# Kernel tuning notes

Hardware: AMD Instinct MI355X
Metric: run time of the kernel (lower is better)

The kernel has to match this reference:

```python
import jax, jax.numpy as jnp
import numpy as np

VOCAB = 50000
D = 32            # hidden_size
OUT = 5           # output_size (sentiment classes)
B = 512           # number of balanced trees
L = 64            # leaves per tree (power of 2)


def setup_inputs() -> dict:
    key = jax.random.key(0)
    ks = jax.random.split(key, 6)
    # scale params down to avoid tanh saturation (original uses xavier init)
    return {
        "word_ids": jax.random.randint(ks[0], (B, L), 0, VOCAB, dtype=jnp.int32),
        "embed": jax.random.normal(ks[1], (VOCAB, D), jnp.float32) * 0.1,
        "V": jax.random.normal(ks[2], (D, 2 * D, 2 * D), jnp.float32) * 0.02,
        "W": jax.random.normal(ks[3], (2 * D, D), jnp.float32) * 0.1,
        "b": jnp.zeros((1, D), jnp.float32),
        "Wout_w": jax.random.normal(ks[4], (OUT, D), jnp.float32) * 0.1,
        "Wout_b": jnp.zeros((OUT,), jnp.float32),
    }


def reference(word_ids, embed, V, W, b, Wout_w, Wout_b):
    # Leaves: embedding lookup. h: [B, n_nodes_at_level, D]
    h = embed[word_ids]                              # [B, L, D]
    all_nodes = [h.reshape(-1, D)]
    n_levels = int(np.log2(h.shape[1]))
    for _ in range(n_levels):
        left = h[:, 0::2]                            # [B, n/2, D]
        right = h[:, 1::2]                           # [B, n/2, D]
        c = jnp.concatenate([left, right], axis=-1)  # [B, n/2, 2D]
        # xVx_k = c @ V_k @ c^T for each slice k of the tensor V
        Vc = jnp.einsum('kjl,bnl->bnkj', V, c)       # [B, n/2, D, 2D]
        xVx = jnp.einsum('bnj,bnkj->bnk', c, Vc)     # [B, n/2, D]
        h = jnp.tanh(xVx + c @ W + b)                # [B, n/2, D]
        all_nodes.append(h.reshape(-1, D))
    nodes = jnp.concatenate(all_nodes, axis=0)       # [B*(2L-1), D]
    logits = nodes @ Wout_w.T + Wout_b               # [B*(2L-1), OUT]
    log_probs = jax.nn.log_softmax(logits, axis=-1)
    roots = h[:, 0, :]                               # [B, D]
    return log_probs, roots
```

## Files before the change

kernel.cpp:

```cpp
#include <hip/hip_runtime.h>

#define OUT_N 5
#define TOTAL_NODES 65024
#define ROOTS_OFF (TOTAL_NODES * OUT_N)

typedef __attribute__((ext_vector_type(8))) short bf16x8;
typedef __attribute__((ext_vector_type(4))) float f32x4;
typedef __attribute__((ext_vector_type(8))) unsigned short ushort8v;
typedef __attribute__((ext_vector_type(4))) unsigned int uint4v;

constexpr int B_BYTES   = 137216;
constexpr int NODE_SZ   = 16128;
constexpr int LEAF_SZ   = 8192;
constexpr int LDS_BIG   = B_BYTES + NODE_SZ + LEAF_SZ;
constexpr int LDS_SMALL = NODE_SZ + LEAF_SZ;

static __device__ __forceinline__ float bf2f(unsigned short u) {
    union { unsigned int i; float f; } v; v.i = ((unsigned int)u) << 16; return v.f;
}
static __device__ __forceinline__ unsigned short f2bf(float f) {
    union { float f; unsigned int i; } v; v.f = f;
    unsigned int r = v.i + 0x7fff + ((v.i >> 16) & 1);
    return (unsigned short)(r >> 16);
}

static __device__ __forceinline__ int naddr32(int R, int c) {
    return R * 128 + (((c + R + (R >> 1)) & 7) << 4);
}
static __device__ __forceinline__ int laddr16(int R, int q) {
    return R * 64 + (((q + R + (R >> 1)) & 3) << 4);
}
static __device__ __forceinline__ void store_h32(char* base, int R, int col, float v) {
    *(float*)(base + naddr32(R, col >> 2) + (col & 3) * 4) = v;
}
static __device__ __forceinline__ void load_crot32(
    const char* base, int Rc, int hi, float* crot)
{
    #pragma unroll
    for (int t = 0; t < 16; ++t) {
        int m = (hi * 2 + t) & 15;
        f32x4 v = *(const f32x4*)(base + naddr32(Rc + (m >> 3), m & 7));
        #pragma unroll
        for (int e = 0; e < 4; ++e) crot[t * 4 + e] = v[e];
    }
}

__global__ __launch_bounds__(64) void bprep_kernel(
    const float* __restrict__ V, const float* __restrict__ W,
    unsigned short* __restrict__ B)
{
    int t = blockIdx.x * 64 + threadIdx.x;
    if (t >= 8576) return;
    int ks = t >> 7, sub = t & 127;
    int n = sub >> 6, lane = sub & 63;
    int hi = lane >> 4, l15 = lane & 15;
    int k = n * 16 + l15;
    const float* Vk = V + (size_t)k * 4096;
    ushort8v o;
    #pragma unroll
    for (int i = 0; i < 8; ++i) {
        int r5 = hi * 8 + i;
        float val;
        if (ks < 2)        { int j = 32 * ks + r5; val = Vk[j * 64 + j]; }
        else if (ks < 64)  { int d = ks >> 1; int j = 32 * (ks & 1) + r5; int l = (j + d) & 63;
                             val = Vk[j * 64 + l] + Vk[l * 64 + j]; }
        else if (ks == 64) { int j = r5; val = Vk[j * 64 + j + 32] + Vk[(j + 32) * 64 + j]; }
        else               { int j = (ks == 65) ? r5 : (32 + r5); val = W[j * 32 + k]; }
        o[i] = f2bf(val);
    }
    *(ushort8v*)(B + (size_t)t * 8) = o;
}

template<int BLDS, int K0, int K1>
static __device__ __forceinline__ f32x4 run1(
    const unsigned short* __restrict__ Bg, const float* crot,
    int lane, int n, f32x4 acc)
{
    extern __shared__ char smem[];
    const int lo = lane * 16 + (n << 10);
    #pragma unroll
    for (int ks = K0; ks < K1; ++ks) {
        uint4v aw;
        #pragma unroll
        for (int q = 0; q < 4; ++q) {
            int i0 = 2 * q, i1 = 2 * q + 1;
            float p0, p1;
            if (ks < 2)       { p0 = crot[32*ks+i0] * crot[32*ks+i0];
                                p1 = crot[32*ks+i1] * crot[32*ks+i1]; }
            else if (ks < 64) { const int bse = 32 * (ks & 1), d = ks >> 1;
                                p0 = crot[bse+i0] * crot[(bse+i0+d)&63];
                                p1 = crot[bse+i1] * crot[(bse+i1+d)&63]; }
            else if (ks == 64){ p0 = crot[i0] * crot[32+i0];
                                p1 = crot[i1] * crot[32+i1]; }
            else if (ks == 65){ p0 = crot[i0];    p1 = crot[i1]; }
            else              { p0 = crot[32+i0]; p1 = crot[32+i1]; }
            unsigned int pk;
            asm("v_cvt_pk_bf16_f32 %0, %1, %2" : "=v"(pk) : "v"(p0), "v"(p1));
            aw[q] = pk;
        }
        bf16x8 afr = __builtin_bit_cast(bf16x8, aw);
        bf16x8 b;
        if constexpr (BLDS) b = *(const bf16x8*)(smem + (ks << 11) + lo);
        else                b = *(const bf16x8*)((const char*)Bg + (ks << 11) + lo);
        acc = __builtin_amdgcn_mfma_f32_16x16x32_bf16(afr, b, acc, 0, 0, 0);
    }
    return acc;
}

template<int BLDS>
static __device__ __attribute__((noinline)) void worker_l1(
    const unsigned short* __restrict__ Bg, const float* __restrict__ bias, int tid)
{
    extern __shared__ char smem[];
    constexpr int NODE = BLDS ? B_BYTES : 0;
    constexpr int LEAF = NODE + NODE_SZ;
    const int lane = tid & 63, w = tid >> 6;
    const int l15 = lane & 15, hi = lane >> 4;
    const int tile = w >> 1, n = w & 1;
    const int tree = tile >> 1, half = tile & 1;

    const int Rc = tree * 64 + half * 32 + 2 * l15;
    float crot[64];
    #pragma unroll
    for (int t = 0; t < 8; ++t) {
        int m = (hi + t) & 7;
        ushort8v v = *(const ushort8v*)(smem + LEAF + laddr16(Rc + (m >> 2), m & 3));
        #pragma unroll
        for (int e = 0; e < 8; ++e) crot[t * 8 + e] = bf2f(v[e]);
    }

    f32x4 a = {0.f,0.f,0.f,0.f};
    a = run1<BLDS, 0, 67>(Bg, crot, lane, n, a);

    float bk = bias[n * 16 + l15];
    #pragma unroll
    for (int r = 0; r < 4; ++r) {
        int R = tree * 63 + half * 16 + hi * 4 + r;
        store_h32(smem + NODE, R, n * 16 + l15, tanhf(a[r] + bk));
    }
    __syncthreads();
}

template<int BLDS>
static __device__ __attribute__((noinline)) void worker_l2(
    const unsigned short* __restrict__ Bg, const float* __restrict__ bias, int tid)
{
    extern __shared__ char smem[];
    constexpr int NODE = BLDS ? B_BYTES : 0;
    constexpr int SCR  = NODE + NODE_SZ;
    const int lane = tid & 63, w = tid >> 6;
    const int l15 = lane & 15, hi = lane >> 4;
    const int tree = w >> 2, n = (w >> 1) & 1, u = w & 1;

    float crot[64];
    load_crot32(smem + NODE, tree * 63 + 2 * l15, hi, crot);

    f32x4 a = {0.f,0.f,0.f,0.f};
    if (u == 0) a = run1<BLDS,  0, 34>(Bg, crot, lane, n, a);
    else        a = run1<BLDS, 34, 67>(Bg, crot, lane, n, a);

    if (u == 1) *(f32x4*)(smem + SCR + ((tree * 2 + n) << 10) + lane * 16) = a;
    __syncthreads();
    if (u == 0) {
        a += *(const f32x4*)(smem + SCR + ((tree * 2 + n) << 10) + lane * 16);
        float bk = bias[n * 16 + l15];
        #pragma unroll
        for (int r = 0; r < 4; ++r) {
            int R = tree * 63 + 32 + hi * 4 + r;
            store_h32(smem + NODE, R, n * 16 + l15, tanhf(a[r] + bk));
        }
    }
    __syncthreads();
}

template<int BLDS>
static __device__ __attribute__((noinline)) void worker_deep(
    const unsigned short* __restrict__ Bg, const float* __restrict__ bias,
    float* __restrict__ roots, int bid, int tid,
    int s, int childb, int outb, bool root)
{
    extern __shared__ char smem[];
    constexpr int NODE = BLDS ? B_BYTES : 0;
    constexpr int SCR  = NODE + NODE_SZ;
    const int lane = tid & 63, w = tid >> 6;
    const int l15 = lane & 15, hi = lane >> 4;
    const int n = w >> 2, u = w & 3;
    const int rptT = 1 << s, rows2 = 2 << s;

    int rc = (l15 < rows2) ? l15 : 0;
    int tree = rc >> s, i = rc & (rptT - 1);
    float crot[64];
    load_crot32(smem + NODE, tree * 63 + childb + 2 * i, hi, crot);

    f32x4 a = {0.f,0.f,0.f,0.f};
    switch (u) {
        case 0:  a = run1<BLDS,  0, 17>(Bg, crot, lane, n, a); break;
        case 1:  a = run1<BLDS, 17, 34>(Bg, crot, lane, n, a); break;
        case 2:  a = run1<BLDS, 34, 50>(Bg, crot, lane, n, a); break;
        default: a = run1<BLDS, 50, 67>(Bg, crot, lane, n, a); break;
    }
    if (u > 0) *(f32x4*)(smem + SCR + ((n * 3 + u - 1) << 10) + lane * 16) = a;
    __syncthreads();
    if (u == 0) {
        #pragma unroll
        for (int v2 = 0; v2 < 3; ++v2)
            a += *(const f32x4*)(smem + SCR + ((n * 3 + v2) << 10) + lane * 16);
        float bk = bias[n * 16 + l15];
        #pragma unroll
        for (int r = 0; r < 4; ++r) {
            int row = hi * 4 + r;
            if (row < rows2) {
                int t2 = row >> s, i2 = row & (rptT - 1);
                float h = tanhf(a[r] + bk);
                store_h32(smem + NODE, t2 * 63 + outb + i2, n * 16 + l15, h);
                if (root) roots[(size_t)(bid * 2 + t2) * 32 + n * 16 + l15] = h;
            }
        }
    }
    __syncthreads();
}

static __device__ __forceinline__ void node_logits32(
    const char* nodebase, int R, const float* __restrict__ Wout_w,
    const float* __restrict__ Wout_b, float* __restrict__ out, size_t g)
{
    float h[32];
    #pragma unroll
    for (int c = 0; c < 8; ++c) {
        f32x4 v = *(const f32x4*)(nodebase + naddr32(R, c));
        #pragma unroll
        for (int e = 0; e < 4; ++e) h[c * 4 + e] = v[e];
    }
    float lg[OUT_N];
    #pragma unroll
    for (int o = 0; o < OUT_N; ++o) {
        const float* ww = Wout_w + o * 32;
        float s = 0.f;
        #pragma unroll
        for (int x = 0; x < 32; ++x) s = fmaf(ww[x], h[x], s);
        lg[o] = s + Wout_b[o];
    }
    float m = lg[0];
    #pragma unroll
    for (int o = 1; o < OUT_N; ++o) m = fmaxf(m, lg[o]);
    float sum = 0.f;
    #pragma unroll
    for (int o = 0; o < OUT_N; ++o) sum += expf(lg[o] - m);
    float lse = m + logf(sum);
    #pragma unroll
    for (int o = 0; o < OUT_N; ++o) out[g * OUT_N + o] = lg[o] - lse;
}

template<int BLDS>
__global__ __launch_bounds__(512, 2) void tree_kernel(
    const int* __restrict__ word_ids, const float* __restrict__ embed,
    const unsigned short* __restrict__ Bg, const float* __restrict__ bias,
    const float* __restrict__ Wout_w, const float* __restrict__ Wout_b,
    float* __restrict__ out)
{
    extern __shared__ char smem[];
    constexpr int NODE = BLDS ? B_BYTES : 0;
    constexpr int LEAF = NODE + NODE_SZ;
    const int tid = threadIdx.x, bid = blockIdx.x;
    float* roots = out + ROOTS_OFF;

    if constexpr (BLDS) {
        const ushort8v* src = (const ushort8v*)Bg;
        #pragma unroll
        for (int r2 = 0; r2 < 16; ++r2) {
            int idx = r2 * 512 + tid;
            *(ushort8v*)(smem + idx * 16) = src[idx];
        }
        int idx = 8192 + tid;
        if (idx < 8576) *(ushort8v*)(smem + idx * 16) = src[idx];
    }

    {
        int rr = tid >> 2, q4 = tid & 3;
        int leaf = bid * 128 + rr;
        int wid = word_ids[leaf];
        const f32x4* ep = (const f32x4*)(embed + (size_t)wid * 32) + q4 * 2;
        f32x4 v0 = ep[0], v1 = ep[1];
        ushort8v o;
        #pragma unroll
        for (int e = 0; e < 4; ++e) { o[e] = f2bf(v0[e]); o[4 + e] = f2bf(v1[e]); }
        *(ushort8v*)(smem + LEAF + laddr16(rr, q4)) = o;

        float lg[OUT_N];
        #pragma unroll
        for (int o5 = 0; o5 < OUT_N; ++o5) {
            const float* ww = Wout_w + o5 * 32 + q4 * 8;
            lg[o5] = ww[0]*v0[0] + ww[1]*v0[1] + ww[2]*v0[2] + ww[3]*v0[3]
                   + ww[4]*v1[0] + ww[5]*v1[1] + ww[6]*v1[2] + ww[7]*v1[3];
        }
        #pragma unroll
        for (int o5 = 0; o5 < OUT_N; ++o5) {
            lg[o5] += __shfl_xor(lg[o5], 1, 64);
            lg[o5] += __shfl_xor(lg[o5], 2, 64);
        }
        if (q4 == 0) {
            #pragma unroll
            for (int o5 = 0; o5 < OUT_N; ++o5) lg[o5] += Wout_b[o5];
            float m = lg[0];
            #pragma unroll
            for (int o5 = 1; o5 < OUT_N; ++o5) m = fmaxf(m, lg[o5]);
            float sum = 0.f;
            #pragma unroll
            for (int o5 = 0; o5 < OUT_N; ++o5) sum += expf(lg[o5] - m);
            float lse = m + logf(sum);
            #pragma unroll
            for (int o5 = 0; o5 < OUT_N; ++o5)
                out[(size_t)leaf * OUT_N + o5] = lg[o5] - lse;
        }
    }
    __syncthreads();

    worker_l1<BLDS>(Bg, bias, tid);
    worker_l2<BLDS>(Bg, bias, tid);
    worker_deep<BLDS>(Bg, bias, roots, bid, tid, 3, 32, 48, false);
    worker_deep<BLDS>(Bg, bias, roots, bid, tid, 2, 48, 56, false);
    worker_deep<BLDS>(Bg, bias, roots, bid, tid, 1, 56, 60, false);
    worker_deep<BLDS>(Bg, bias, roots, bid, tid, 0, 60, 62, true);

    if (tid < 126) {
        int tree = (tid >= 63) ? 1 : 0;
        int r = tid - 63 * tree;
        size_t tg = (size_t)bid * 2 + tree;
        int R = tree * 63 + r;
        size_t g;
        if (r < 32)      g = 32768 + tg * 32 + r;
        else if (r < 48) g = 49152 + tg * 16 + (r - 32);
        else if (r < 56) g = 57344 + tg * 8  + (r - 48);
        else if (r < 60) g = 61440 + tg * 4  + (r - 56);
        else if (r < 62) g = 63488 + tg * 2  + (r - 60);
        else             g = 64512 + tg;
        node_logits32(smem + NODE, R, Wout_w, Wout_b, out, g);
    }
}

extern "C" void kernel_launch(void* const* d_in, const int* in_sizes, int n_in,
                              void* d_out, int out_size, void* d_ws, size_t ws_size,
                              hipStream_t stream)
{
    const int*   word_ids = (const int*)  d_in[0];
    const float* embed    = (const float*)d_in[1];
    const float* V        = (const float*)d_in[2];
    const float* W        = (const float*)d_in[3];
    const float* bvec     = (const float*)d_in[4];
    const float* Wout_w   = (const float*)d_in[5];
    const float* Wout_b   = (const float*)d_in[6];
    float* out = (float*)d_out;

    unsigned short* Bfrag = (unsigned short*)d_ws;

    bprep_kernel<<<134, 64, 0, stream>>>(V, W, Bfrag);

    hipError_t e = hipFuncSetAttribute((const void*)&tree_kernel<1>,
                     hipFuncAttributeMaxDynamicSharedMemorySize, LDS_BIG);
    if (e == hipSuccess) {
        tree_kernel<1><<<256, 512, LDS_BIG, stream>>>(
            word_ids, embed, Bfrag, bvec, Wout_w, Wout_b, out);
    } else {
        tree_kernel<0><<<256, 512, LDS_SMALL, stream>>>(
            word_ids, embed, Bfrag, bvec, Wout_w, Wout_b, out);
    }
}
```

Measured before the change: 31.15 us.

## Double tree-kernel block size and stage V slices through LDS in bprep

Launches the tree kernel with 1024 threads instead of 512. Level 1 now splits its K range across two waves and reduces partials through LDS scratch, while the deeper levels leave the extra waves idle. The bprep kernel now loads each V_k slice into shared memory with coalesced reads before building the fragments, and the leaf embedding gather is spread over 8 lanes per leaf. The global-memory fallback path is removed, so the kernel now depends on the large LDS allocation succeeding. Idle waves in the deep levels add barrier cost, and the added split adds an extra synchronisation.

```diff
diff --git a/kernel.cpp b/kernel.cpp
--- a/kernel.cpp
+++ b/kernel.cpp
@@ -9,11 +9,13 @@
 typedef __attribute__((ext_vector_type(8))) unsigned short ushort8v;
 typedef __attribute__((ext_vector_type(4))) unsigned int uint4v;
 
-constexpr int B_BYTES   = 137216;
-constexpr int NODE_SZ   = 16128;
-constexpr int LEAF_SZ   = 8192;
-constexpr int LDS_BIG   = B_BYTES + NODE_SZ + LEAF_SZ;
-constexpr int LDS_SMALL = NODE_SZ + LEAF_SZ;
+constexpr int B_BYTES = 137216;
+constexpr int NODE_SZ = 16128;
+constexpr int LEAF_SZ = 8192;
+constexpr int NODE = B_BYTES;
+constexpr int LEAF = NODE + NODE_SZ;
+constexpr int SCR  = LEAF;
+constexpr int LDS_BIG = B_BYTES + NODE_SZ + LEAF_SZ;
 
 static __device__ __forceinline__ float bf2f(unsigned short u) {
     union { unsigned int i; float f; } v; v.i = ((unsigned int)u) << 16; return v.f;
@@ -45,36 +47,41 @@
     }
 }
 
-__global__ __launch_bounds__(64) void bprep_kernel(
+__global__ __launch_bounds__(256) void bprep_kernel(
     const float* __restrict__ V, const float* __restrict__ W,
     unsigned short* __restrict__ B)
 {
-    int t = blockIdx.x * 64 + threadIdx.x;
-    if (t >= 8576) return;
-    int ks = t >> 7, sub = t & 127;
-    int n = sub >> 6, lane = sub & 63;
-    int hi = lane >> 4, l15 = lane & 15;
-    int k = n * 16 + l15;
-    const float* Vk = V + (size_t)k * 4096;
-    ushort8v o;
-    #pragma unroll
-    for (int i = 0; i < 8; ++i) {
-        int r5 = hi * 8 + i;
-        float val;
-        if (ks < 2)        { int j = 32 * ks + r5; val = Vk[j * 64 + j]; }
-        else if (ks < 64)  { int d = ks >> 1; int j = 32 * (ks & 1) + r5; int l = (j + d) & 63;
-                             val = Vk[j * 64 + l] + Vk[l * 64 + j]; }
-        else if (ks == 64) { int j = r5; val = Vk[j * 64 + j + 32] + Vk[(j + 32) * 64 + j]; }
-        else               { int j = (ks == 65) ? r5 : (32 + r5); val = W[j * 32 + k]; }
-        o[i] = f2bf(val);
-    }
-    *(ushort8v*)(B + (size_t)t * 8) = o;
-}
-
-template<int BLDS, int K0, int K1>
+    __shared__ float vk[4096];
+    const int tid = threadIdx.x, k = blockIdx.x;
+    #pragma unroll
+    for (int i = 0; i < 4; ++i) {
+        int idx = i * 256 + tid;
+        ((f32x4*)vk)[idx] = ((const f32x4*)(V + (size_t)k * 4096))[idx];
+    }
+    __syncthreads();
+    const int n = k >> 4, l15 = k & 15;
+    for (int jb = tid; jb < 268; jb += 256) {
+        int ks = jb % 67, hi4 = jb / 67;
+        ushort8v o;
+        #pragma unroll
+        for (int i = 0; i < 8; ++i) {
+            int r5 = hi4 * 8 + i;
+            float val;
+            if (ks < 2)        { int j = 32 * ks + r5; val = vk[j * 64 + j]; }
+            else if (ks < 64)  { int d = ks >> 1; int j = 32 * (ks & 1) + r5;
+                                 int l = (j + d) & 63;
+                                 val = vk[j * 64 + l] + vk[l * 64 + j]; }
+            else if (ks == 64) { int j = r5; val = vk[j * 64 + j + 32] + vk[(j + 32) * 64 + j]; }
+            else               { int j = (ks == 65) ? r5 : (32 + r5); val = W[j * 32 + k]; }
+            o[i] = f2bf(val);
+        }
+        *(ushort8v*)(B + (size_t)(ks * 128 + n * 64 + hi4 * 16 + l15) * 8) = o;
+    }
+}
+
+template<int K0, int K1>
 static __device__ __forceinline__ f32x4 run1(
-    const unsigned short* __restrict__ Bg, const float* crot,
-    int lane, int n, f32x4 acc)
+    const float* crot, int lane, int n, f32x4 acc)
 {
     extern __shared__ char smem[];
     const int lo = lane * 16 + (n << 10);
@@ -99,69 +106,99 @@
             aw[q] = pk;
         }
         bf16x8 afr = __builtin_bit_cast(bf16x8, aw);
-        bf16x8 b;
-        if constexpr (BLDS) b = *(const bf16x8*)(smem + (ks << 11) + lo);
-        else                b = *(const bf16x8*)((const char*)Bg + (ks << 11) + lo);
+        bf16x8 b = *(const bf16x8*)(smem + (ks << 11) + lo);
         acc = __builtin_amdgcn_mfma_f32_16x16x32_bf16(afr, b, acc, 0, 0, 0);
     }
     return acc;
 }
 
-template<int BLDS>
+static __device__ __forceinline__ void node_logits32(
+    const char* nodebase, int R, const float* __restrict__ Wout_w,
+    const float* __restrict__ Wout_b, float* __restrict__ out, size_t g)
+{
+    float h[32];
+    #pragma unroll
+    for (int c = 0; c < 8; ++c) {
+        f32x4 v = *(const f32x4*)(nodebase + naddr32(R, c));
+        #pragma unroll
+        for (int e = 0; e < 4; ++e) h[c * 4 + e] = v[e];
+    }
+    float lg[OUT_N];
+    #pragma unroll
+    for (int o = 0; o < OUT_N; ++o) {
+        const float* ww = Wout_w + o * 32;
+        float s = 0.f;
+        #pragma unroll
+        for (int x = 0; x < 32; ++x) s = fmaf(ww[x], h[x], s);
+        lg[o] = s + Wout_b[o];
+    }
+    float m = lg[0];
+    #pragma unroll
+    for (int o = 1; o < OUT_N; ++o) m = fmaxf(m, lg[o]);
+    float sum = 0.f;
+    #pragma unroll
+    for (int o = 0; o < OUT_N; ++o) sum += expf(lg[o] - m);
+    float lse = m + logf(sum);
+    #pragma unroll
+    for (int o = 0; o < OUT_N; ++o) out[g * OUT_N + o] = lg[o] - lse;
+}
+
 static __device__ __attribute__((noinline)) void worker_l1(
-    const unsigned short* __restrict__ Bg, const float* __restrict__ bias, int tid)
-{
-    extern __shared__ char smem[];
-    constexpr int NODE = BLDS ? B_BYTES : 0;
-    constexpr int LEAF = NODE + NODE_SZ;
+    const float* __restrict__ bias, int tid)
+{
+    extern __shared__ char smem[];
     const int lane = tid & 63, w = tid >> 6;
     const int l15 = lane & 15, hi = lane >> 4;
-    const int tile = w >> 1, n = w & 1;
-    const int tree = tile >> 1, half = tile & 1;
+    const int t = w >> 2, n = (w >> 1) & 1, u = w & 1;
+    const int tree = t >> 1, half = t & 1;
 
     const int Rc = tree * 64 + half * 32 + 2 * l15;
     float crot[64];
     #pragma unroll
-    for (int t = 0; t < 8; ++t) {
-        int m = (hi + t) & 7;
+    for (int tt = 0; tt < 8; ++tt) {
+        int m = (hi + tt) & 7;
         ushort8v v = *(const ushort8v*)(smem + LEAF + laddr16(Rc + (m >> 2), m & 3));
         #pragma unroll
-        for (int e = 0; e < 8; ++e) crot[t * 8 + e] = bf2f(v[e]);
-    }
+        for (int e = 0; e < 8; ++e) crot[tt * 8 + e] = bf2f(v[e]);
+    }
+    __syncthreads();
 
     f32x4 a = {0.f,0.f,0.f,0.f};
-    a = run1<BLDS, 0, 67>(Bg, crot, lane, n, a);
-
-    float bk = bias[n * 16 + l15];
-    #pragma unroll
-    for (int r = 0; r < 4; ++r) {
-        int R = tree * 63 + half * 16 + hi * 4 + r;
-        store_h32(smem + NODE, R, n * 16 + l15, tanhf(a[r] + bk));
-    }
-    __syncthreads();
-}
-
-template<int BLDS>
+    if (u == 0) a = run1< 0, 34>(crot, lane, n, a);
+    else        a = run1<34, 67>(crot, lane, n, a);
+
+    if (u == 1) *(f32x4*)(smem + SCR + ((t * 2 + n) << 10) + lane * 16) = a;
+    __syncthreads();
+    if (u == 0) {
+        a += *(const f32x4*)(smem + SCR + ((t * 2 + n) << 10) + lane * 16);
+        float bk = bias[n * 16 + l15];
+        #pragma unroll
+        for (int r = 0; r < 4; ++r) {
+            int R = tree * 63 + half * 16 + hi * 4 + r;
+            store_h32(smem + NODE, R, n * 16 + l15, tanhf(a[r] + bk));
+        }
+    }
+    __syncthreads();
+}
+
 static __device__ __attribute__((noinline)) void worker_l2(
-    const unsigned short* __restrict__ Bg, const float* __restrict__ bias, int tid)
-{
-    extern __shared__ char smem[];
-    constexpr int NODE = BLDS ? B_BYTES : 0;
-    constexpr int SCR  = NODE + NODE_SZ;
+    const float* __restrict__ bias, int tid)
+{
+    extern __shared__ char smem[];
     const int lane = tid & 63, w = tid >> 6;
     const int l15 = lane & 15, hi = lane >> 4;
-    const int tree = w >> 2, n = (w >> 1) & 1, u = w & 1;
-
-    float crot[64];
-    load_crot32(smem + NODE, tree * 63 + 2 * l15, hi, crot);
+    const int tree = (w >> 2) & 1, n = (w >> 1) & 1, u = w & 1;
 
     f32x4 a = {0.f,0.f,0.f,0.f};
-    if (u == 0) a = run1<BLDS,  0, 34>(Bg, crot, lane, n, a);
-    else        a = run1<BLDS, 34, 67>(Bg, crot, lane, n, a);
-
-    if (u == 1) *(f32x4*)(smem + SCR + ((tree * 2 + n) << 10) + lane * 16) = a;
-    __syncthreads();
-    if (u == 0) {
+    if (w < 8) {
+        float crot[64];
+        load_crot32(smem + NODE, tree * 63 + 2 * l15, hi, crot);
+        if (u == 0) a = run1< 0, 34>(crot, lane, n, a);
+        else        a = run1<34, 67>(crot, lane, n, a);
+        if (u == 1) *(f32x4*)(smem + SCR + ((tree * 2 + n) << 10) + lane * 16) = a;
+    }
+    __syncthreads();
+    if (w < 8 && u == 0) {
         a += *(const f32x4*)(smem + SCR + ((tree * 2 + n) << 10) + lane * 16);
         float bk = bias[n * 16 + l15];
         #pragma unroll
@@ -173,35 +210,32 @@
     __syncthreads();
 }
 
-template<int BLDS>
 static __device__ __attribute__((noinline)) void worker_deep(
-    const unsigned short* __restrict__ Bg, const float* __restrict__ bias,
-    float* __restrict__ roots, int bid, int tid,
-    int s, int childb, int outb, bool root)
-{
-    extern __shared__ char smem[];
-    constexpr int NODE = BLDS ? B_BYTES : 0;
-    constexpr int SCR  = NODE + NODE_SZ;
+    const float* __restrict__ bias, float* __restrict__ roots,
+    int bid, int tid, int s, int childb, int outb, bool root)
+{
+    extern __shared__ char smem[];
     const int lane = tid & 63, w = tid >> 6;
     const int l15 = lane & 15, hi = lane >> 4;
-    const int n = w >> 2, u = w & 3;
+    const int n = (w >> 2) & 1, u = w & 3;
     const int rptT = 1 << s, rows2 = 2 << s;
 
-    int rc = (l15 < rows2) ? l15 : 0;
-    int tree = rc >> s, i = rc & (rptT - 1);
-    float crot[64];
-    load_crot32(smem + NODE, tree * 63 + childb + 2 * i, hi, crot);
-
     f32x4 a = {0.f,0.f,0.f,0.f};
-    switch (u) {
-        case 0:  a = run1<BLDS,  0, 17>(Bg, crot, lane, n, a); break;
-        case 1:  a = run1<BLDS, 17, 34>(Bg, crot, lane, n, a); break;
-        case 2:  a = run1<BLDS, 34, 50>(Bg, crot, lane, n, a); break;
-        default: a = run1<BLDS, 50, 67>(Bg, crot, lane, n, a); break;
-    }
-    if (u > 0) *(f32x4*)(smem + SCR + ((n * 3 + u - 1) << 10) + lane * 16) = a;
-    __syncthreads();
-    if (u == 0) {
+    if (w < 8) {
+        int rc = (l15 < rows2) ? l15 : 0;
+        int tree = rc >> s, i = rc & (rptT - 1);
+        float crot[64];
+        load_crot32(smem + NODE, tree * 63 + childb + 2 * i, hi, crot);
+        switch (u) {
+            case 0:  a = run1< 0, 17>(crot, lane, n, a); break;
+            case 1:  a = run1<17, 34>(crot, lane, n, a); break;
+            case 2:  a = run1<34, 50>(crot, lane, n, a); break;
+            default: a = run1<50, 67>(crot, lane, n, a); break;
+        }
+        if (u > 0) *(f32x4*)(smem + SCR + ((n * 3 + u - 1) << 10) + lane * 16) = a;
+    }
+    __syncthreads();
+    if (w < 8 && u == 0) {
         #pragma unroll
         for (int v2 = 0; v2 < 3; ++v2)
             a += *(const f32x4*)(smem + SCR + ((n * 3 + v2) << 10) + lane * 16);
@@ -220,55 +254,21 @@
     __syncthreads();
 }
 
-static __device__ __forceinline__ void node_logits32(
-    const char* nodebase, int R, const float* __restrict__ Wout_w,
-    const float* __restrict__ Wout_b, float* __restrict__ out, size_t g)
-{
-    float h[32];
-    #pragma unroll
-    for (int c = 0; c < 8; ++c) {
-        f32x4 v = *(const f32x4*)(nodebase + naddr32(R, c));
-        #pragma unroll
-        for (int e = 0; e < 4; ++e) h[c * 4 + e] = v[e];
-    }
-    float lg[OUT_N];
-    #pragma unroll
-    for (int o = 0; o < OUT_N; ++o) {
-        const float* ww = Wout_w + o * 32;
-        float s = 0.f;
-        #pragma unroll
-        for (int x = 0; x < 32; ++x) s = fmaf(ww[x], h[x], s);
-        lg[o] = s + Wout_b[o];
-    }
-    float m = lg[0];
-    #pragma unroll
-    for (int o = 1; o < OUT_N; ++o) m = fmaxf(m, lg[o]);
-    float sum = 0.f;
-    #pragma unroll
-    for (int o = 0; o < OUT_N; ++o) sum += expf(lg[o] - m);
-    float lse = m + logf(sum);
-    #pragma unroll
-    for (int o = 0; o < OUT_N; ++o) out[g * OUT_N + o] = lg[o] - lse;
-}
-
-template<int BLDS>
-__global__ __launch_bounds__(512, 2) void tree_kernel(
+__global__ __launch_bounds__(1024, 2) void tree_kernel(
     const int* __restrict__ word_ids, const float* __restrict__ embed,
     const unsigned short* __restrict__ Bg, const float* __restrict__ bias,
     const float* __restrict__ Wout_w, const float* __restrict__ Wout_b,
     float* __restrict__ out)
 {
     extern __shared__ char smem[];
-    constexpr int NODE = BLDS ? B_BYTES : 0;
-    constexpr int LEAF = NODE + NODE_SZ;
     const int tid = threadIdx.x, bid = blockIdx.x;
     float* roots = out + ROOTS_OFF;
 
-    if constexpr (BLDS) {
+    {
         const ushort8v* src = (const ushort8v*)Bg;
         #pragma unroll
-        for (int r2 = 0; r2 < 16; ++r2) {
-            int idx = r2 * 512 + tid;
+        for (int r2 = 0; r2 < 8; ++r2) {
+            int idx = r2 * 1024 + tid;
             *(ushort8v*)(smem + idx * 16) = src[idx];
         }
         int idx = 8192 + tid;
@@ -276,27 +276,26 @@
     }
 
     {
-        int rr = tid >> 2, q4 = tid & 3;
+        int rr = tid >> 3, q4 = tid & 7;
         int leaf = bid * 128 + rr;
         int wid = word_ids[leaf];
-        const f32x4* ep = (const f32x4*)(embed + (size_t)wid * 32) + q4 * 2;
-        f32x4 v0 = ep[0], v1 = ep[1];
-        ushort8v o;
-        #pragma unroll
-        for (int e = 0; e < 4; ++e) { o[e] = f2bf(v0[e]); o[4 + e] = f2bf(v1[e]); }
-        *(ushort8v*)(smem + LEAF + laddr16(rr, q4)) = o;
+        f32x4 v = ((const f32x4*)(embed + (size_t)wid * 32))[q4];
+        uint2 st;
+        st.x = (unsigned)f2bf(v[0]) | ((unsigned)f2bf(v[1]) << 16);
+        st.y = (unsigned)f2bf(v[2]) | ((unsigned)f2bf(v[3]) << 16);
+        *(uint2*)(smem + LEAF + laddr16(rr, q4 >> 1) + (q4 & 1) * 8) = st;
 
         float lg[OUT_N];
         #pragma unroll
         for (int o5 = 0; o5 < OUT_N; ++o5) {
-            const float* ww = Wout_w + o5 * 32 + q4 * 8;
-            lg[o5] = ww[0]*v0[0] + ww[1]*v0[1] + ww[2]*v0[2] + ww[3]*v0[3]
-                   + ww[4]*v1[0] + ww[5]*v1[1] + ww[6]*v1[2] + ww[7]*v1[3];
+            const float* ww = Wout_w + o5 * 32 + q4 * 4;
+            lg[o5] = ww[0]*v[0] + ww[1]*v[1] + ww[2]*v[2] + ww[3]*v[3];
         }
         #pragma unroll
         for (int o5 = 0; o5 < OUT_N; ++o5) {
             lg[o5] += __shfl_xor(lg[o5], 1, 64);
             lg[o5] += __shfl_xor(lg[o5], 2, 64);
+            lg[o5] += __shfl_xor(lg[o5], 4, 64);
         }
         if (q4 == 0) {
             #pragma unroll
@@ -315,12 +314,12 @@
     }
     __syncthreads();
 
-    worker_l1<BLDS>(Bg, bias, tid);
-    worker_l2<BLDS>(Bg, bias, tid);
-    worker_deep<BLDS>(Bg, bias, roots, bid, tid, 3, 32, 48, false);
-    worker_deep<BLDS>(Bg, bias, roots, bid, tid, 2, 48, 56, false);
-    worker_deep<BLDS>(Bg, bias, roots, bid, tid, 1, 56, 60, false);
-    worker_deep<BLDS>(Bg, bias, roots, bid, tid, 0, 60, 62, true);
+    worker_l1(bias, tid);
+    worker_l2(bias, tid);
+    worker_deep(bias, roots, bid, tid, 3, 32, 48, false);
+    worker_deep(bias, roots, bid, tid, 2, 48, 56, false);
+    worker_deep(bias, roots, bid, tid, 1, 56, 60, false);
+    worker_deep(bias, roots, bid, tid, 0, 60, 62, true);
 
     if (tid < 126) {
         int tree = (tid >= 63) ? 1 : 0;
@@ -353,15 +352,10 @@
 
     unsigned short* Bfrag = (unsigned short*)d_ws;
 
-    bprep_kernel<<<134, 64, 0, stream>>>(V, W, Bfrag);
-
-    hipError_t e = hipFuncSetAttribute((const void*)&tree_kernel<1>,
-                     hipFuncAttributeMaxDynamicSharedMemorySize, LDS_BIG);
-    if (e == hipSuccess) {
-        tree_kernel<1><<<256, 512, LDS_BIG, stream>>>(
-            word_ids, embed, Bfrag, bvec, Wout_w, Wout_b, out);
-    } else {
-        tree_kernel<0><<<256, 512, LDS_SMALL, stream>>>(
-            word_ids, embed, Bfrag, bvec, Wout_w, Wout_b, out);
-    }
-}
+    bprep_kernel<<<32, 256, 0, stream>>>(V, W, Bfrag);
+
+    (void)hipFuncSetAttribute((const void*)&tree_kernel,
+            hipFuncAttributeMaxDynamicSharedMemorySize, LDS_BIG);
+    tree_kernel<<<256, 1024, LDS_BIG, stream>>>(
+        word_ids, embed, Bfrag, bvec, Wout_w, Wout_b, out);
+}
```

Measured after the change: 31.95 us. +2.6%, slower.
